# Kernel optimization log

Hardware: AMD Instinct MI355X
Metric: run time of the kernel (lower is better)

The kernel has to match this reference:

```python
import jax, jax.numpy as jnp
import numpy as np

MAXDISP = 320
NEG_SLOPE = 0.2


def _lrelu(x):
    return jnp.where(x >= 0, x, NEG_SLOPE * x)


def _conv(x, w, b, stride):
    # NCHW conv, VALID padding (torch Conv2d with padding=0)
    y = jax.lax.conv_general_dilated(x, w, window_strides=stride, padding='VALID',
                                     dimension_numbers=('NCHW', 'OIHW', 'NCHW'))
    return y + b[None, :, None, None]


def _tile_pair(fl, fr, wa, ba, wb, bb):
    # left: 4x4 conv stride (4,4); right: ZeroPad2d((0,3,0,0)) then stride (4,1)
    tl = _lrelu(_conv(_lrelu(_conv(fl, wa, ba, (4, 4))), wb, bb, (1, 1)))
    frp = jnp.pad(fr, ((0, 0), (0, 0), (0, 0), (0, 3)))
    tr = _lrelu(_conv(_lrelu(_conv(frp, wa, ba, (4, 1))), wb, bb, (1, 1)))
    return tl, tr


def _calc_init_disp(fl, fr, D):
    # fl: [B,C,h,w4], fr: [B,C,h,w] with w = 4*w4.
    # grid_sample(nearest, align_corners=True) with integer coords reduces to
    # exact gather at right column index 4*j - d, zero outside (padding_mode=zeros).
    B, C, h, w4 = fl.shape
    w = fr.shape[3]
    j = jnp.arange(w4)
    d = jnp.arange(D)
    idx = 4 * j[None, :] - d[:, None]              # [D, w4]
    valid = idx >= 0                               # only left edge can go OOB
    idxc = jnp.clip(idx, 0, w - 1)
    fr_g = fr[:, :, :, idxc]                       # [B,C,h,D,w4]
    fr_g = jnp.where(valid[None, None, None, :, :], fr_g, jnp.zeros((), fr.dtype))
    cv = jnp.abs(fl[:, :, :, None, :] - fr_g).sum(axis=1)  # L1 over C -> [B,h,D,w4]
    return jnp.transpose(cv, (0, 2, 1, 3))         # [B,D,h,w4]


def _level_hyp(cv, dscrpt_feat, dw, db):
    min_cost = jnp.min(cv, axis=1, keepdims=True)
    disp = jnp.argmin(cv, axis=1, keepdims=True).astype(cv.dtype)
    dscrpt = _lrelu(_conv(jnp.concatenate([min_cost, dscrpt_feat], axis=1), dw, db, (1, 1)))
    z = jnp.zeros_like(disp)
    return jnp.concatenate([disp, z, z, dscrpt], axis=1)  # [B,16,h,w]


def setup_inputs() -> dict:
    key = jax.random.key(0)
    ks = iter(jax.random.split(key, 64))

    def rn(shape, s=1.0):
        return jax.random.normal(next(ks), shape, dtype=jnp.float32) * s

    B, H, W = 1, 384, 1280
    inp = {
        'fea_l16': rn((B, 32, H // 16, W // 16)), 'fea_l8': rn((B, 24, H // 8, W // 8)),
        'fea_l4': rn((B, 24, H // 4, W // 4)), 'fea_l2': rn((B, 16, H // 2, W // 2)),
        'fea_l1': rn((B, 16, H, W)),
        'fea_r16': rn((B, 32, H // 16, W // 16)), 'fea_r8': rn((B, 24, H // 8, W // 8)),
        'fea_r4': rn((B, 24, H // 4, W // 4)), 'fea_r2': rn((B, 16, H // 2, W // 2)),
        'fea_r1': rn((B, 16, H, W)),
    }
    fea_c = {16: 32, 8: 24, 4: 24, 2: 16, 1: 16}
    for s, c in fea_c.items():
        inp[f'tcw{s}a'] = rn((16, c, 4, 4), 0.1)
        inp[f'tcb{s}a'] = rn((16,), 0.1)
        inp[f'tcw{s}b'] = rn((16, 16, 1, 1), 0.1)
        inp[f'tcb{s}b'] = rn((16,), 0.1)
    dsc_in = {16: 17, 8: 17, 4: 33, 2: 25, 1: 25}
    for s, c in dsc_in.items():
        inp[f'dw{s}'] = rn((13, c, 1, 1), 0.1)
        inp[f'db{s}'] = rn((13,), 0.1)
    return inp


def reference(fea_l16, fea_l8, fea_l4, fea_l2, fea_l1,
              fea_r16, fea_r8, fea_r4, fea_r2, fea_r1,
              tcw16a, tcb16a, tcw16b, tcb16b,
              tcw8a, tcb8a, tcw8b, tcb8b,
              tcw4a, tcb4a, tcw4b, tcb4b,
              tcw2a, tcb2a, tcw2b, tcb2b,
              tcw1a, tcb1a, tcw1b, tcb1b,
              dw16, db16, dw8, db8, dw4, db4, dw2, db2, dw1, db1):
    tl16, tr16 = _tile_pair(fea_l16, fea_r16, tcw16a, tcb16a, tcw16b, tcb16b)
    tl8, tr8 = _tile_pair(fea_l8, fea_r8, tcw8a, tcb8a, tcw8b, tcb8b)
    tl4, tr4 = _tile_pair(fea_l4, fea_r4, tcw4a, tcb4a, tcw4b, tcb4b)
    tl2, tr2 = _tile_pair(fea_l2, fea_r2, tcw2a, tcb2a, tcw2b, tcb2b)
    tl1, tr1 = _tile_pair(fea_l1, fea_r1, tcw1a, tcb1a, tcw1b, tcb1b)

    cv16 = _calc_init_disp(tl16, tr16, MAXDISP // 16)
    cv8 = _calc_init_disp(tl8, tr8, MAXDISP // 8)
    cv4 = _calc_init_disp(tl4, tr4, MAXDISP // 4)
    cv2 = _calc_init_disp(tl2, tr2, MAXDISP // 2)
    cv1 = _calc_init_disp(tl1, tr1, MAXDISP)

    hyp16 = _level_hyp(cv16, tl16, dw16, db16)
    hyp8 = _level_hyp(cv8, tl8, dw8, db8)
    hyp4 = _level_hyp(cv4, fea_l16, dw4, db4)
    hyp2 = _level_hyp(cv2, fea_l8, dw2, db2)
    hyp1 = _level_hyp(cv1, fea_l4, dw1, db1)

    return (cv16, cv8, cv4, cv2, cv1, hyp16, hyp8, hyp4, hyp2, hyp1)
```

## Files before the change

kernel.cpp:

```cpp
#include <hip/hip_runtime.h>
#include <float.h>

#define NEG_SLOPE 0.2f

__device__ __forceinline__ float lrelu(float x) { return x >= 0.0f ? x : NEG_SLOPE * x; }

struct ConvSeg {
    const float* in; const float* wa; const float* ba; const float* wb; const float* bb;
    float* out;
    int CIN, H, W, SX, OW, npix, blk0;
};
struct ConvTab { ConvSeg seg[10]; };

__global__ __launch_bounds__(256)
void conv_uber(ConvTab tab) {
    __shared__ float s_wa[32 * 256];
    __shared__ float s_wb[256];
    __shared__ float s_ba[16], s_bb[16];
    __shared__ float s_part[16 * 256];
    __shared__ float s_m[16 * 64];

    int si = 0;
#pragma unroll
    for (int i = 1; i < 10; i++) if ((int)blockIdx.x >= tab.seg[i].blk0) si = i;
    const ConvSeg sg = tab.seg[si];
    const int CIN = sg.CIN;

    for (int i = threadIdx.x; i < CIN * 256; i += 256)
        s_wa[i] = sg.wa[(i & 15) * (CIN * 16) + (i >> 4)];
    {
        int i = threadIdx.x;
        s_wb[i] = sg.wb[(i & 15) * 16 + (i >> 4)];
        if (i < 16) { s_ba[i] = sg.ba[i]; s_bb[i] = sg.bb[i]; }
    }
    __syncthreads();

    const int p = threadIdx.x & 63, chunk = threadIdx.x >> 6;
    const int pix = ((int)blockIdx.x - sg.blk0) * 64 + p;
    const bool valid = pix < sg.npix;

    float m[16];
#pragma unroll
    for (int co = 0; co < 16; co++) m[co] = 0.f;

    const int cpc = CIN >> 2;
    if (valid) {
        int y = pix / sg.OW, x = pix - y * sg.OW;
        int c0 = chunk * cpc;
        if (sg.SX == 4) {
            for (int c = c0; c < c0 + cpc; c++) {
                const float* rb = sg.in + ((size_t)(c * sg.H + 4 * y)) * sg.W + 4 * x;
                const float* wc = &s_wa[c * 256];
#pragma unroll
                for (int r = 0; r < 4; r++) {
                    float4 v = *(const float4*)(rb + r * sg.W);
                    const float* wr = wc + r * 64;
#pragma unroll
                    for (int co = 0; co < 16; co++) m[co] = fmaf(v.x, wr[co], m[co]);
#pragma unroll
                    for (int co = 0; co < 16; co++) m[co] = fmaf(v.y, wr[16 + co], m[co]);
#pragma unroll
                    for (int co = 0; co < 16; co++) m[co] = fmaf(v.z, wr[32 + co], m[co]);
#pragma unroll
                    for (int co = 0; co < 16; co++) m[co] = fmaf(v.w, wr[48 + co], m[co]);
                }
            }
        } else {
            for (int c = c0; c < c0 + cpc; c++) {
                const float* wc = &s_wa[c * 256];
#pragma unroll
                for (int r = 0; r < 4; r++) {
                    const float* rb = sg.in + ((size_t)(c * sg.H + 4 * y + r)) * sg.W;
                    const float* wr = wc + r * 64;
#pragma unroll
                    for (int kx = 0; kx < 4; kx++) {
                        int col = x + kx;
                        float v = (col < sg.W) ? rb[col] : 0.f;
                        const float* w2 = wr + kx * 16;
#pragma unroll
                        for (int co = 0; co < 16; co++) m[co] = fmaf(v, w2[co], m[co]);
                    }
                }
            }
        }
    }
#pragma unroll
    for (int co = 0; co < 16; co++) s_part[co * 256 + threadIdx.x] = m[co];
    __syncthreads();

#pragma unroll
    for (int i = 0; i < 4; i++) {
        int co = chunk * 4 + i;
        float v = s_part[co * 256 + p] + s_part[co * 256 + 64 + p]
                + s_part[co * 256 + 128 + p] + s_part[co * 256 + 192 + p];
        s_m[co * 64 + p] = lrelu(v + s_ba[co]);
    }
    __syncthreads();

    float o[4] = {0.f, 0.f, 0.f, 0.f};
#pragma unroll
    for (int k = 0; k < 16; k++) {
        float mk = s_m[k * 64 + p];
        const float* wr = &s_wb[k * 16 + chunk * 4];
#pragma unroll
        for (int i = 0; i < 4; i++) o[i] = fmaf(mk, wr[i], o[i]);
    }
    if (valid) {
#pragma unroll
        for (int i = 0; i < 4; i++) {
            int co = chunk * 4 + i;
            sg.out[(size_t)co * sg.npix + pix] = lrelu(o[i] + s_bb[co]);
        }
    }
}

struct CvSeg {
    const float* tl; const float* tr; const float* feat;
    const float* dw; const float* db;
    float* cv; float* hyp;
    int h, w4, w, D, gpc, CF, blk0;
};
struct CvTab { CvSeg seg[5]; };

__global__ __launch_bounds__(256)
void cv_hyp_uber(CvTab tab) {
    __shared__ float smin[256];
    __shared__ int sarg[256];

    int si = 0;
#pragma unroll
    for (int i = 1; i < 5; i++) if ((int)blockIdx.x >= tab.seg[i].blk0) si = i;
    const CvSeg sg = tab.seg[si];

    const int npix = sg.h * sg.w4;
    const int p = threadIdx.x & 63, chunk = threadIdx.x >> 6;
    const int pix = ((int)blockIdx.x - sg.blk0) * 64 + p;
    const bool valid = pix < npix;

    float mloc = FLT_MAX; int aloc = 0;
    if (valid) {
        int y = pix / sg.w4, j = pix - y * sg.w4;
        float tlv[16]; float sumabs = 0.f;
#pragma unroll
        for (int c = 0; c < 16; c++) { tlv[c] = sg.tl[(size_t)c * npix + pix]; sumabs += fabsf(tlv[c]); }

        int ngroups = sg.D >> 2;
        int g0 = chunk * sg.gpc;
        int g1 = min(ngroups, g0 + sg.gpc);
        const float* trrow = sg.tr + (size_t)y * sg.w;
        int hw = sg.h * sg.w;

        float carry[16];
        int b0 = 4 * j - 4 * g0;
        if (g0 < g1 && b0 >= 0) {
#pragma unroll
            for (int c = 0; c < 16; c++) carry[c] = trrow[(size_t)c * hw + b0];
        }
        for (int g = g0; g < g1; g++) {
            int b = 4 * j - 4 * g;
            float a0, a1, a2, a3;
            if (b >= 4) {
                a0 = a1 = a2 = a3 = 0.f;
#pragma unroll
                for (int c = 0; c < 16; c++) {
                    float4 f0 = *(const float4*)(trrow + (size_t)c * hw + (b - 4));
                    float tv = tlv[c];
                    a0 += fabsf(tv - carry[c]);
                    a1 += fabsf(tv - f0.w);
                    a2 += fabsf(tv - f0.z);
                    a3 += fabsf(tv - f0.y);
                    carry[c] = f0.x;
                }
            } else if (b == 0) {
                a0 = 0.f; a1 = a2 = a3 = sumabs;
#pragma unroll
                for (int c = 0; c < 16; c++) a0 += fabsf(tlv[c] - carry[c]);
            } else {
                a0 = a1 = a2 = a3 = sumabs;
            }
            float* cvp = sg.cv + (size_t)(4 * g) * npix + pix;
            cvp[0] = a0; cvp[npix] = a1; cvp[2 * (size_t)npix] = a2; cvp[3 * (size_t)npix] = a3;
            if (a0 < mloc) { mloc = a0; aloc = 4 * g; }
            if (a1 < mloc) { mloc = a1; aloc = 4 * g + 1; }
            if (a2 < mloc) { mloc = a2; aloc = 4 * g + 2; }
            if (a3 < mloc) { mloc = a3; aloc = 4 * g + 3; }
        }
    }
    smin[threadIdx.x] = mloc;
    sarg[threadIdx.x] = aloc;
    __syncthreads();

    if (threadIdx.x < 64 && valid) {
        float mn = smin[threadIdx.x]; int arg = sarg[threadIdx.x];
#pragma unroll
        for (int c2 = 1; c2 < 4; c2++) {
            float v = smin[c2 * 64 + threadIdx.x];
            if (v < mn) { mn = v; arg = sarg[c2 * 64 + threadIdx.x]; }
        }
        float acc[13];
#pragma unroll
        for (int o = 0; o < 13; o++) acc[o] = sg.dw[o * (sg.CF + 1)] * mn;
        for (int c = 0; c < sg.CF; c++) {
            float v = sg.feat[(size_t)c * npix + pix];
#pragma unroll
            for (int o = 0; o < 13; o++) acc[o] = fmaf(v, sg.dw[o * (sg.CF + 1) + 1 + c], acc[o]);
        }
        sg.hyp[pix] = (float)arg;
        sg.hyp[npix + pix] = 0.f;
        sg.hyp[2 * (size_t)npix + pix] = 0.f;
#pragma unroll
        for (int o = 0; o < 13; o++) sg.hyp[(size_t)(3 + o) * npix + pix] = lrelu(acc[o] + sg.db[o]);
    }
}

extern "C" void kernel_launch(void* const* d_in, const int* in_sizes, int n_in,
                              void* d_out, int out_size, void* d_ws, size_t ws_size,
                              hipStream_t stream) {
    (void)in_sizes; (void)n_in; (void)out_size; (void)ws_size;
    float* out = (float*)d_out;
    float* ws = (float*)d_ws;

    const int C[5] = {32, 24, 24, 16, 16};
    const int H[5] = {24, 48, 96, 192, 384};
    const int W[5] = {80, 160, 320, 640, 1280};
    const int D[5] = {20, 40, 80, 160, 320};
    const int wa_i[5] = {10, 14, 18, 22, 26};
    const int dw_i[5] = {30, 32, 34, 36, 38};

    const size_t cv_off[5]  = {0, 2400, 21600, 175200, 1404000};
    const size_t hyp_off[5] = {11234400, 11236320, 11244000, 11274720, 11397600};
    const size_t tl_off[5] = {0, 9600, 48000, 201600, 816000};
    const size_t tr_off[5] = {1920, 17280, 78720, 324480, 1307520};

    const float* fl[5] = {(const float*)d_in[0], (const float*)d_in[1], (const float*)d_in[2],
                          (const float*)d_in[3], (const float*)d_in[4]};
    const float* fr[5] = {(const float*)d_in[5], (const float*)d_in[6], (const float*)d_in[7],
                          (const float*)d_in[8], (const float*)d_in[9]};

    const int ord_lvl[10]  = {4, 4, 3, 3, 2, 2, 1, 1, 0, 0};
    const int ord_side[10] = {1, 0, 1, 0, 1, 0, 1, 0, 1, 0};
    ConvTab ct;
    int blk = 0;
    for (int i = 0; i < 10; i++) {
        int l = ord_lvl[i]; bool right = ord_side[i];
        ConvSeg& s = ct.seg[i];
        s.in = right ? fr[l] : fl[l];
        s.wa = (const float*)d_in[wa_i[l]];
        s.ba = (const float*)d_in[wa_i[l] + 1];
        s.wb = (const float*)d_in[wa_i[l] + 2];
        s.bb = (const float*)d_in[wa_i[l] + 3];
        s.out = ws + (right ? tr_off[l] : tl_off[l]);
        s.CIN = C[l]; s.H = H[l]; s.W = W[l];
        s.SX = right ? 1 : 4;
        s.OW = right ? W[l] : W[l] / 4;
        s.npix = (H[l] / 4) * s.OW;
        s.blk0 = blk;
        blk += (s.npix + 63) / 64;
    }
    conv_uber<<<blk, 256, 0, stream>>>(ct);

    const float* feat[5] = {ws + tl_off[0], ws + tl_off[1], fl[0], fl[1], fl[2]};
    const int   CF[5]    = {16, 16, 32, 24, 24};
    CvTab vt;
    blk = 0;
    for (int i = 0; i < 5; i++) {
        int l = 4 - i;
        CvSeg& s = vt.seg[i];
        s.tl = ws + tl_off[l]; s.tr = ws + tr_off[l];
        s.feat = feat[l];
        s.dw = (const float*)d_in[dw_i[l]];
        s.db = (const float*)d_in[dw_i[l] + 1];
        s.cv = out + cv_off[l]; s.hyp = out + hyp_off[l];
        s.h = H[l] / 4; s.w4 = W[l] / 4; s.w = W[l]; s.D = D[l];
        int ngroups = D[l] / 4;
        s.gpc = (ngroups + 3) / 4;
        s.CF = CF[l];
        s.blk0 = blk;
        blk += (s.h * s.w4 + 63) / 64;
    }
    cv_hyp_uber<<<blk, 256, 0, stream>>>(vt);
}
```

Baseline: 354.2 us.

## Pre-transpose conv weights and compute one pixel per thread without LDS

Adds a small pre-kernel that transposes the conv weights into workspace once per call. The conv kernel then gives each thread a whole pixel across all input channels, instead of splitting channels four ways and reducing through shared memory. It reads weights from global memory (uniform, cache-friendly), drops the per-block weight staging, the partial-sum reduction and the barriers, and uses 256 pixels per block. The cost is a serial loop over all channels per thread, uniform scalar or global weight loads in place of LDS reads, higher register pressure, fewer blocks and an extra launch.

```diff
diff --git a/kernel.cpp b/kernel.cpp
--- a/kernel.cpp
+++ b/kernel.cpp
@@ -5,8 +5,20 @@
 
 __device__ __forceinline__ float lrelu(float x) { return x >= 0.0f ? x : NEG_SLOPE * x; }
 
+struct PrepSeg { const float* wa; const float* wb; float* wat; float* wbt; int CIN; };
+struct PrepTab { PrepSeg seg[5]; };
+
+__global__ __launch_bounds__(256)
+void prep_weights(PrepTab tab) {
+    PrepSeg sg = tab.seg[blockIdx.x];
+    int n = sg.CIN * 256;
+    for (int i = threadIdx.x; i < n; i += 256)
+        sg.wat[i] = sg.wa[(i & 15) * (sg.CIN * 16) + (i >> 4)];
+    sg.wbt[threadIdx.x] = sg.wb[(threadIdx.x & 15) * 16 + (threadIdx.x >> 4)];
+}
+
 struct ConvSeg {
-    const float* in; const float* wa; const float* ba; const float* wb; const float* bb;
+    const float* in; const float* wat; const float* wbt; const float* ba; const float* bb;
     float* out;
     int CIN, H, W, SX, OW, npix, blk0;
 };
@@ -14,103 +26,79 @@
 
 __global__ __launch_bounds__(256)
 void conv_uber(ConvTab tab) {
-    __shared__ float s_wa[32 * 256];
-    __shared__ float s_wb[256];
-    __shared__ float s_ba[16], s_bb[16];
-    __shared__ float s_part[16 * 256];
-    __shared__ float s_m[16 * 64];
-
     int si = 0;
 #pragma unroll
     for (int i = 1; i < 10; i++) if ((int)blockIdx.x >= tab.seg[i].blk0) si = i;
     const ConvSeg sg = tab.seg[si];
-    const int CIN = sg.CIN;
-
-    for (int i = threadIdx.x; i < CIN * 256; i += 256)
-        s_wa[i] = sg.wa[(i & 15) * (CIN * 16) + (i >> 4)];
-    {
-        int i = threadIdx.x;
-        s_wb[i] = sg.wb[(i & 15) * 16 + (i >> 4)];
-        if (i < 16) { s_ba[i] = sg.ba[i]; s_bb[i] = sg.bb[i]; }
-    }
-    __syncthreads();
-
-    const int p = threadIdx.x & 63, chunk = threadIdx.x >> 6;
-    const int pix = ((int)blockIdx.x - sg.blk0) * 64 + p;
+
+    int pix = ((int)blockIdx.x - sg.blk0) * 256 + threadIdx.x;
     const bool valid = pix < sg.npix;
+    int cpix = valid ? pix : sg.npix - 1;
+    int y = cpix / sg.OW, x = cpix - y * sg.OW;
 
     float m[16];
 #pragma unroll
     for (int co = 0; co < 16; co++) m[co] = 0.f;
 
-    const int cpc = CIN >> 2;
-    if (valid) {
-        int y = pix / sg.OW, x = pix - y * sg.OW;
-        int c0 = chunk * cpc;
-        if (sg.SX == 4) {
-            for (int c = c0; c < c0 + cpc; c++) {
-                const float* rb = sg.in + ((size_t)(c * sg.H + 4 * y)) * sg.W + 4 * x;
-                const float* wc = &s_wa[c * 256];
-#pragma unroll
-                for (int r = 0; r < 4; r++) {
-                    float4 v = *(const float4*)(rb + r * sg.W);
-                    const float* wr = wc + r * 64;
-#pragma unroll
-                    for (int co = 0; co < 16; co++) m[co] = fmaf(v.x, wr[co], m[co]);
-#pragma unroll
-                    for (int co = 0; co < 16; co++) m[co] = fmaf(v.y, wr[16 + co], m[co]);
-#pragma unroll
-                    for (int co = 0; co < 16; co++) m[co] = fmaf(v.z, wr[32 + co], m[co]);
-#pragma unroll
-                    for (int co = 0; co < 16; co++) m[co] = fmaf(v.w, wr[48 + co], m[co]);
+    const int W = sg.W, H = sg.H, CIN = sg.CIN;
+    const int xb = (sg.SX == 4) ? 4 * x : x;
+    const bool fast = (sg.SX == 4) || (x + 4 <= W);
+    const float* ib = sg.in + (size_t)(4 * y) * W;
+
+    if (fast) {
+        for (int c = 0; c < CIN; c++) {
+            const float* rb = ib + (size_t)c * H * W + xb;
+            const float* wc = sg.wat + c * 256;
+#pragma unroll
+            for (int r = 0; r < 4; r++) {
+                float4 v = *(const float4*)(rb + r * W);
+                const float* wr = wc + r * 64;
+#pragma unroll
+                for (int co = 0; co < 16; co++) m[co] = fmaf(v.x, wr[co], m[co]);
+#pragma unroll
+                for (int co = 0; co < 16; co++) m[co] = fmaf(v.y, wr[16 + co], m[co]);
+#pragma unroll
+                for (int co = 0; co < 16; co++) m[co] = fmaf(v.z, wr[32 + co], m[co]);
+#pragma unroll
+                for (int co = 0; co < 16; co++) m[co] = fmaf(v.w, wr[48 + co], m[co]);
+            }
+        }
+    } else {
+        for (int c = 0; c < CIN; c++) {
+            const float* rb = ib + (size_t)c * H * W;
+            const float* wc = sg.wat + c * 256;
+#pragma unroll
+            for (int r = 0; r < 4; r++) {
+                const float* wr = wc + r * 64;
+#pragma unroll
+                for (int kx = 0; kx < 4; kx++) {
+                    int col = xb + kx;
+                    float v = (col < W) ? rb[r * W + col] : 0.f;
+                    const float* w2 = wr + kx * 16;
+#pragma unroll
+                    for (int co = 0; co < 16; co++) m[co] = fmaf(v, w2[co], m[co]);
                 }
             }
-        } else {
-            for (int c = c0; c < c0 + cpc; c++) {
-                const float* wc = &s_wa[c * 256];
-#pragma unroll
-                for (int r = 0; r < 4; r++) {
-                    const float* rb = sg.in + ((size_t)(c * sg.H + 4 * y + r)) * sg.W;
-                    const float* wr = wc + r * 64;
-#pragma unroll
-                    for (int kx = 0; kx < 4; kx++) {
-                        int col = x + kx;
-                        float v = (col < sg.W) ? rb[col] : 0.f;
-                        const float* w2 = wr + kx * 16;
-#pragma unroll
-                        for (int co = 0; co < 16; co++) m[co] = fmaf(v, w2[co], m[co]);
-                    }
-                }
-            }
-        }
-    }
-#pragma unroll
-    for (int co = 0; co < 16; co++) s_part[co * 256 + threadIdx.x] = m[co];
-    __syncthreads();
-
-#pragma unroll
-    for (int i = 0; i < 4; i++) {
-        int co = chunk * 4 + i;
-        float v = s_part[co * 256 + p] + s_part[co * 256 + 64 + p]
-                + s_part[co * 256 + 128 + p] + s_part[co * 256 + 192 + p];
-        s_m[co * 64 + p] = lrelu(v + s_ba[co]);
-    }
-    __syncthreads();
-
-    float o[4] = {0.f, 0.f, 0.f, 0.f};
+        }
+    }
+
+#pragma unroll
+    for (int co = 0; co < 16; co++) m[co] = lrelu(m[co] + sg.ba[co]);
+
+    float o[16];
+#pragma unroll
+    for (int co = 0; co < 16; co++) o[co] = 0.f;
 #pragma unroll
     for (int k = 0; k < 16; k++) {
-        float mk = s_m[k * 64 + p];
-        const float* wr = &s_wb[k * 16 + chunk * 4];
-#pragma unroll
-        for (int i = 0; i < 4; i++) o[i] = fmaf(mk, wr[i], o[i]);
+        float mk = m[k];
+        const float* wr = sg.wbt + k * 16;
+#pragma unroll
+        for (int co = 0; co < 16; co++) o[co] = fmaf(mk, wr[co], o[co]);
     }
     if (valid) {
 #pragma unroll
-        for (int i = 0; i < 4; i++) {
-            int co = chunk * 4 + i;
-            sg.out[(size_t)co * sg.npix + pix] = lrelu(o[i] + s_bb[co]);
-        }
+        for (int co = 0; co < 16; co++)
+            sg.out[(size_t)co * sg.npix + pix] = lrelu(o[co] + sg.bb[co]);
     }
 }
 
@@ -231,11 +219,23 @@
     const size_t hyp_off[5] = {11234400, 11236320, 11244000, 11274720, 11397600};
     const size_t tl_off[5] = {0, 9600, 48000, 201600, 816000};
     const size_t tr_off[5] = {1920, 17280, 78720, 324480, 1307520};
+    const size_t wat_off[5] = {3280000, 3288192, 3294336, 3300480, 3304576};
+    const size_t wbt_off[5] = {3310000, 3310256, 3310512, 3310768, 3311024};
 
     const float* fl[5] = {(const float*)d_in[0], (const float*)d_in[1], (const float*)d_in[2],
                           (const float*)d_in[3], (const float*)d_in[4]};
     const float* fr[5] = {(const float*)d_in[5], (const float*)d_in[6], (const float*)d_in[7],
                           (const float*)d_in[8], (const float*)d_in[9]};
+
+    PrepTab pt;
+    for (int l = 0; l < 5; l++) {
+        pt.seg[l].wa = (const float*)d_in[wa_i[l]];
+        pt.seg[l].wb = (const float*)d_in[wa_i[l] + 2];
+        pt.seg[l].wat = ws + wat_off[l];
+        pt.seg[l].wbt = ws + wbt_off[l];
+        pt.seg[l].CIN = C[l];
+    }
+    prep_weights<<<5, 256, 0, stream>>>(pt);
 
     const int ord_lvl[10]  = {4, 4, 3, 3, 2, 2, 1, 1, 0, 0};
     const int ord_side[10] = {1, 0, 1, 0, 1, 0, 1, 0, 1, 0};
@@ -245,9 +245,9 @@
         int l = ord_lvl[i]; bool right = ord_side[i];
         ConvSeg& s = ct.seg[i];
         s.in = right ? fr[l] : fl[l];
-        s.wa = (const float*)d_in[wa_i[l]];
+        s.wat = ws + wat_off[l];
+        s.wbt = ws + wbt_off[l];
         s.ba = (const float*)d_in[wa_i[l] + 1];
-        s.wb = (const float*)d_in[wa_i[l] + 2];
         s.bb = (const float*)d_in[wa_i[l] + 3];
         s.out = ws + (right ? tr_off[l] : tl_off[l]);
         s.CIN = C[l]; s.H = H[l]; s.W = W[l];
@@ -255,7 +255,7 @@
         s.OW = right ? W[l] : W[l] / 4;
         s.npix = (H[l] / 4) * s.OW;
         s.blk0 = blk;
-        blk += (s.npix + 63) / 64;
+        blk += (s.npix + 255) / 256;
     }
     conv_uber<<<blk, 256, 0, stream>>>(ct);
 
```

Result: slower. 366.3 us (+3.4%).
